# Kernel optimization log

Hardware: AMD Instinct MI355X
Metric: run time of the kernel (lower is better)

Reference implementation:

```python
import jax, jax.numpy as jnp
import numpy as np

NU, NI, D, E = 50000, 100000, 128, 500000
UMAX, IMAX = 50, 50
SQRT_D = float(np.sqrt(D))


def seg_softmax(vals, seg, n):
    # numerically stable softmax over edges grouped by segment id (sparse row softmax)
    m = jax.ops.segment_max(vals, seg, num_segments=n)
    ex = jnp.exp(vals - m[seg])
    s = jax.ops.segment_sum(ex, seg, num_segments=n)
    return ex / s[seg]


def setup_inputs() -> dict:
    key = jax.random.key(0)
    ks = jax.random.split(key, 20)
    w = lambda k: jax.random.normal(k, (D, D), dtype=jnp.float32) * 0.05
    return {
        "u_emb": jax.random.normal(ks[0], (NU, D), dtype=jnp.float32),
        "i_emb": jax.random.normal(ks[1], (NI, D), dtype=jnp.float32),
        "edge_u": jax.random.randint(ks[2], (E,), 0, NU),
        "edge_i": jax.random.randint(ks[3], (E,), 0, NI),
        "rui": jax.random.randint(ks[4], (E,), 0, UMAX),
        "riu": jax.random.randint(ks[5], (E,), 0, IMAX),
        "last_u_items": jax.random.randint(ks[6], (NU,), 0, NI),
        "last_i_users": jax.random.randint(ks[7], (NU,), 0, NU),
        "W1": w(ks[8]), "W2": w(ks[9]), "W1b": w(ks[10]), "W2b": w(ks[11]),
        "W3": w(ks[12]), "W4": w(ks[13]),
        "pV": jax.random.normal(ks[14], (UMAX, D), dtype=jnp.float32),
        "pK": jax.random.normal(ks[15], (IMAX, D), dtype=jnp.float32),
        "last_user_table": jax.random.normal(ks[16], (NU, D), dtype=jnp.float32),
        "last_item_table": jax.random.normal(ks[17], (NI, D), dtype=jnp.float32),
    }


def reference(u_emb, i_emb, edge_u, edge_i, rui, riu, last_u_items, last_i_users,
              W1, W2, W1b, W2b, W3, W4, pV, pK, last_user_table, last_item_table):
    # nn.Linear: y = x @ W.T
    um = u_emb @ W2.T            # (NU, D) user messages
    im = i_emb @ W1.T            # (NI, D) item messages
    um_e = um[edge_u]            # (E, D) gathered per edge
    im_e = im[edge_i]            # (E, D)

    # ---- long term ----
    # dense e = um @ im.T masked to edges == per-edge dot products (same math)
    e_vals = jnp.sum(um_e * im_e, axis=-1)                     # (E,)
    pVui = pV[rui]                                             # (E, D)
    pKiu = pK[riu]                                             # (E, D)
    e_ui = e_vals + jnp.sum(um_e * pVui, axis=-1)
    e_iu = e_vals + jnp.sum(im_e * pKiu, axis=-1)
    alphas = seg_softmax(e_ui / SQRT_D, edge_u, NU)            # softmax over items per user
    betas = seg_softmax(e_iu / SQRT_D, edge_i, NI)             # softmax over users per item

    umb = u_emb @ W2b.T
    imb = i_emb @ W1b.T
    # pass_messages: out[row] = sum_e alpha_e * (messages[col_e] + p_e)
    hLu = jax.ops.segment_sum(alphas[:, None] * (imb[edge_i] + pKiu), edge_u, num_segments=NU)
    hLi = jax.ops.segment_sum(betas[:, None] * (umb[edge_u] + pVui), edge_i, num_segments=NI)

    # ---- short term ----
    li = last_item_table[last_u_items] @ W3.T                  # (NU, D)
    lu = last_user_table[last_i_users] @ W4.T                  # (NU, D)
    a_vals = jnp.sum(li[edge_u] * im_e, axis=-1)               # (E,)
    b_vals = jnp.sum(lu[edge_u] * im_e, axis=-1)               # (E,)
    alphas_s = seg_softmax(a_vals / SQRT_D, edge_u, NU)
    betas_s = seg_softmax(b_vals / SQRT_D, edge_i, NI)
    # p = ones -> messages + 1
    hSu = jax.ops.segment_sum(alphas_s[:, None] * (im_e + 1.0), edge_u, num_segments=NU)
    hSi = jax.ops.segment_sum(betas_s[:, None] * (um_e + 1.0), edge_i, num_segments=NI)

    return (hLu, hSu, hLi, hSi)
```

## Files before the change

### kernel.cpp

```cpp
#include <hip/hip_runtime.h>
#include <hip/hip_bf16.h>
#include <math.h>

#define D_ 128
#define INV_SQRT_D 0.08838834764831845f
#define SCAN_CH 16
#define SCAN_TILE (256 * SCAN_CH)

typedef __bf16 bf16x8 __attribute__((ext_vector_type(8)));
typedef float f32x4 __attribute__((ext_vector_type(4)));

struct W4p { const float* p[4]; };

__device__ __forceinline__ void unpack8(bf16x8 v, float* f) {
    const uint32_t* u = (const uint32_t*)&v;
#pragma unroll
    for (int i = 0; i < 4; i++) {
        uint32_t w = u[i];
        f[2 * i]     = __uint_as_float(w << 16);
        f[2 * i + 1] = __uint_as_float(w & 0xffff0000u);
    }
}

__device__ __forceinline__ bf16x8 pack8(const float* f, float s) {
    bf16x8 r;
#pragma unroll
    for (int j = 0; j < 8; j++) r[j] = (__bf16)(f[j] * s);
    return r;
}

__global__ __launch_bounds__(256) void cvt_weights4(W4p w, __bf16* __restrict__ out) {
    int idx = blockIdx.x * 256 + threadIdx.x;
    if (idx >= 4 * 16384) return;
    out[idx] = (__bf16)w.p[idx >> 14][idx & 16383];
}

__global__ __launch_bounds__(256) void cvt2(const float* __restrict__ a, const float* __restrict__ b,
                                            __bf16* __restrict__ oa, __bf16* __restrict__ ob, int n) {
    int idx = blockIdx.x * 256 + threadIdx.x;
    if (idx < n) { oa[idx] = (__bf16)a[idx]; ob[idx] = (__bf16)b[idx]; }
}

__global__ __launch_bounds__(256) void cvt_emb(const float* __restrict__ u, const float* __restrict__ i,
                                               __bf16* __restrict__ ub, __bf16* __restrict__ ib,
                                               size_t nue, size_t nie) {
    size_t idx4 = ((size_t)blockIdx.x * 256 + threadIdx.x) * 4;
    if (idx4 < nue) {
        float4 v = *(const float4*)(u + idx4);
        ub[idx4] = (__bf16)v.x; ub[idx4+1] = (__bf16)v.y; ub[idx4+2] = (__bf16)v.z; ub[idx4+3] = (__bf16)v.w;
    } else if (idx4 < nue + nie) {
        size_t j = idx4 - nue;
        float4 v = *(const float4*)(i + j);
        ib[j] = (__bf16)v.x; ib[j+1] = (__bf16)v.y; ib[j+2] = (__bf16)v.z; ib[j+3] = (__bf16)v.w;
    }
}

__global__ __launch_bounds__(128) void prep_mats(const float* __restrict__ W1, const float* __restrict__ W2,
                                                 const float* __restrict__ W3, const float* __restrict__ W4,
                                                 const float* __restrict__ pV, const float* __restrict__ pK,
                                                 __bf16* __restrict__ M2t, __bf16* __restrict__ M3t,
                                                 __bf16* __restrict__ M4t,
                                                 __bf16* __restrict__ pVW2, __bf16* __restrict__ pKW1,
                                                 int umax, int imax) {
    __shared__ float sh[256];
    int b = blockIdx.x, t = threadIdx.x;
    if (b < 128) {
        sh[t] = W1[t * 128 + b];
        __syncthreads();
        float m2 = 0.f, m3 = 0.f, m4 = 0.f;
        for (int k = 0; k < 128; k++) {
            float w = sh[k];
            m2 = fmaf(w, W2[k * 128 + t], m2);
            m3 = fmaf(w, W3[k * 128 + t], m3);
            m4 = fmaf(w, W4[k * 128 + t], m4);
        }
        M2t[b * 128 + t] = (__bf16)(m2 * INV_SQRT_D);
        M3t[b * 128 + t] = (__bf16)(m3 * INV_SQRT_D);
        M4t[b * 128 + t] = (__bf16)(m4 * INV_SQRT_D);
    } else {
        int r = b - 128;
        if (r < umax) sh[t] = pV[r * 128 + t];
        if (r < imax) sh[128 + t] = pK[r * 128 + t];
        __syncthreads();
        float q = 0.f, qk = 0.f;
        for (int a = 0; a < 128; a++) {
            if (r < umax) q  = fmaf(sh[a], W2[a * 128 + t], q);
            if (r < imax) qk = fmaf(sh[128 + a], W1[a * 128 + t], qk);
        }
        if (r < umax) pVW2[r * 128 + t] = (__bf16)(q * INV_SQRT_D);
        if (r < imax) pKW1[r * 128 + t] = (__bf16)(qk * INV_SQRT_D);
    }
}

__global__ __launch_bounds__(256) void user_vecs(const float* __restrict__ u_emb,
                                                 const float* __restrict__ lit_tab, const int* __restrict__ g_li,
                                                 const float* __restrict__ lut_tab, const int* __restrict__ g_lu,
                                                 const __bf16* __restrict__ M2t, const __bf16* __restrict__ M3t,
                                                 const __bf16* __restrict__ M4t,
                                                 __bf16* __restrict__ um_t, __bf16* __restrict__ li_t,
                                                 __bf16* __restrict__ lu_t, int rows) {
    int lane = threadIdx.x & 63;
    int wave = threadIdx.x >> 6;
    int row0 = blockIdx.x * 64 + wave * 16;
    if (row0 >= rows) return;
    int l16 = lane & 15, kh = lane >> 4;
    int ar = row0 + l16;
    int arc = ar < rows ? ar : rows - 1;
    const float* rA = u_emb + (size_t)arc * D_;
    const float* rB = lit_tab + (size_t)g_li[arc] * D_;
    const float* rC = lut_tab + (size_t)g_lu[arc] * D_;

    f32x4 aA[8] = {}, aB[8] = {}, aC[8] = {};
#pragma unroll
    for (int k0 = 0; k0 < D_; k0 += 32) {
        int kk = k0 + kh * 8;
        float4 a0 = *(const float4*)(rA + kk), a1 = *(const float4*)(rA + kk + 4);
        float4 b0 = *(const float4*)(rB + kk), b1 = *(const float4*)(rB + kk + 4);
        float4 c0 = *(const float4*)(rC + kk), c1 = *(const float4*)(rC + kk + 4);
        bf16x8 fA, fB, fC;
        fA[0]=(__bf16)a0.x; fA[1]=(__bf16)a0.y; fA[2]=(__bf16)a0.z; fA[3]=(__bf16)a0.w;
        fA[4]=(__bf16)a1.x; fA[5]=(__bf16)a1.y; fA[6]=(__bf16)a1.z; fA[7]=(__bf16)a1.w;
        fB[0]=(__bf16)b0.x; fB[1]=(__bf16)b0.y; fB[2]=(__bf16)b0.z; fB[3]=(__bf16)b0.w;
        fB[4]=(__bf16)b1.x; fB[5]=(__bf16)b1.y; fB[6]=(__bf16)b1.z; fB[7]=(__bf16)b1.w;
        fC[0]=(__bf16)c0.x; fC[1]=(__bf16)c0.y; fC[2]=(__bf16)c0.z; fC[3]=(__bf16)c0.w;
        fC[4]=(__bf16)c1.x; fC[5]=(__bf16)c1.y; fC[6]=(__bf16)c1.z; fC[7]=(__bf16)c1.w;
#pragma unroll
        for (int cb = 0; cb < 8; cb++) {
            bf16x8 w2 = *(const bf16x8*)(M2t + (size_t)(cb * 16 + l16) * D_ + kk);
            aA[cb] = __builtin_amdgcn_mfma_f32_16x16x32_bf16(fA, w2, aA[cb], 0, 0, 0);
            bf16x8 w3 = *(const bf16x8*)(M3t + (size_t)(cb * 16 + l16) * D_ + kk);
            aB[cb] = __builtin_amdgcn_mfma_f32_16x16x32_bf16(fB, w3, aB[cb], 0, 0, 0);
            bf16x8 w4 = *(const bf16x8*)(M4t + (size_t)(cb * 16 + l16) * D_ + kk);
            aC[cb] = __builtin_amdgcn_mfma_f32_16x16x32_bf16(fC, w4, aC[cb], 0, 0, 0);
        }
    }
#pragma unroll
    for (int cb = 0; cb < 8; cb++) {
#pragma unroll
        for (int j = 0; j < 4; j++) {
            int r = row0 + kh * 4 + j;
            if (r < rows) {
                um_t[(size_t)r * D_ + cb * 16 + l16] = (__bf16)aA[cb][j];
                li_t[(size_t)r * D_ + cb * 16 + l16] = (__bf16)aB[cb][j];
                lu_t[(size_t)r * D_ + cb * 16 + l16] = (__bf16)aC[cb][j];
            }
        }
    }
}

__global__ __launch_bounds__(256) void gemm_pvk(const __bf16* __restrict__ Xb,
                                                const __bf16* __restrict__ Pb,
                                                float* __restrict__ Y, int rows, int ncols) {
    int lane = threadIdx.x & 63;
    int wave = threadIdx.x >> 6;
    int row0 = blockIdx.x * 64 + wave * 16;
    if (row0 >= rows) return;
    int l16 = lane & 15, kh = lane >> 4;
    int ar = row0 + l16;
    int arc = ar < rows ? ar : rows - 1;
    const __bf16* arow = Xb + (size_t)arc * D_;

    f32x4 acc[4] = {};
#pragma unroll
    for (int k0 = 0; k0 < D_; k0 += 32) {
        int kk = k0 + kh * 8;
        bf16x8 af = *(const bf16x8*)(arow + kk);
#pragma unroll
        for (int cb = 0; cb < 4; cb++) {
            int br = cb * 16 + l16;
            if (br >= ncols) br = ncols - 1;
            bf16x8 bf = *(const bf16x8*)(Pb + (size_t)br * D_ + kk);
            acc[cb] = __builtin_amdgcn_mfma_f32_16x16x32_bf16(af, bf, acc[cb], 0, 0, 0);
        }
    }
#pragma unroll
    for (int cb = 0; cb < 4; cb++) {
        int col = cb * 16 + l16;
        if (col >= ncols) continue;
#pragma unroll
        for (int j = 0; j < 4; j++) {
            int r = row0 + kh * 4 + j;
            if (r < rows) Y[(size_t)r * ncols + col] = acc[cb][j];
        }
    }
}

__global__ __launch_bounds__(256) void hist2(const int* __restrict__ eu, const int* __restrict__ ei,
                                             int* __restrict__ cnt_all, int nu, int E) {
    int e = blockIdx.x * 256 + threadIdx.x;
    if (e < E) {
        atomicAdd(&cnt_all[eu[e]], 1);
        atomicAdd(&cnt_all[nu + ei[e]], 1);
    }
}

__global__ __launch_bounds__(256) void scan_phaseA(const int* __restrict__ cnt, int* __restrict__ part, int n) {
    __shared__ int wsum[4];
    int t = threadIdx.x, lane = t & 63, w = t >> 6;
    int i0 = blockIdx.x * SCAN_TILE + t * SCAN_CH;
    int tot = 0;
#pragma unroll
    for (int j = 0; j < SCAN_CH; j++) tot += (i0 + j < n) ? cnt[i0 + j] : 0;
#pragma unroll
    for (int d = 32; d; d >>= 1) tot += __shfl_xor(tot, d);
    if (lane == 0) wsum[w] = tot;
    __syncthreads();
    if (t == 0) part[blockIdx.x] = wsum[0] + wsum[1] + wsum[2] + wsum[3];
}

__global__ __launch_bounds__(1024) void scan_phaseB(int* __restrict__ part, int nb,
                                                    int* __restrict__ off, int n) {
    __shared__ int wsum[16];
    int t = threadIdx.x, lane = t & 63, w = t >> 6;
    int v = (t < nb) ? part[t] : 0;
    int x = v;
#pragma unroll
    for (int d = 1; d < 64; d <<= 1) {
        int y = __shfl_up(x, d);
        if (lane >= d) x += y;
    }
    if (lane == 63) wsum[w] = x;
    __syncthreads();
    int wbase = 0;
    for (int ww = 0; ww < w; ww++) wbase += wsum[ww];
    if (t < nb) part[t] = wbase + x - v;
    if (t == 1023) off[n] = wbase + x;
}

__global__ __launch_bounds__(256) void scan_phaseC(const int* __restrict__ cnt, const int* __restrict__ part,
                                                   int* __restrict__ off, int* __restrict__ pos, int n) {
    __shared__ int wsum[4];
    int t = threadIdx.x, lane = t & 63, w = t >> 6;
    int i0 = blockIdx.x * SCAN_TILE + t * SCAN_CH;
    int loc[SCAN_CH];
    int tot = 0;
#pragma unroll
    for (int j = 0; j < SCAN_CH; j++) {
        int v = (i0 + j < n) ? cnt[i0 + j] : 0;
        loc[j] = tot; tot += v;
    }
    int x = tot;
#pragma unroll
    for (int d = 1; d < 64; d <<= 1) {
        int y = __shfl_up(x, d);
        if (lane >= d) x += y;
    }
    if (lane == 63) wsum[w] = x;
    __syncthreads();
    int wbase = 0;
    for (int ww = 0; ww < w; ww++) wbase += wsum[ww];
    int excl = part[blockIdx.x] + wbase + x - tot;
#pragma unroll
    for (int j = 0; j < SCAN_CH; j++) {
        if (i0 + j < n) { off[i0 + j] = excl + loc[j]; pos[i0 + j] = excl + loc[j]; }
    }
}

__global__ __launch_bounds__(256) void scatter2(const int* __restrict__ eu, const int* __restrict__ ei,
                                                const int* __restrict__ rui, const int* __restrict__ riu,
                                                int* __restrict__ pos_all, int4* __restrict__ recs,
                                                int nu, int E) {
    int e = blockIdx.x * 256 + threadIdx.x;
    if (e < E) {
        int u = eu[e], it = ei[e], r1 = rui[e], r2 = riu[e];
        int pi = atomicAdd(&pos_all[nu + it], 1);
        int pu = atomicAdd(&pos_all[u], 1);
        recs[pu] = make_int4(it, r1, r2, pi);
        recs[pi] = make_int4(u, r1, r2, 0);
    }
}

__global__ __launch_bounds__(256) void user_pass(const int* __restrict__ off_all, const int4* __restrict__ recs,
                                                 const __bf16* __restrict__ ib_emb,
                                                 const __bf16* __restrict__ um_t,
                                                 const __bf16* __restrict__ li_t,
                                                 const __bf16* __restrict__ lu_t,
                                                 const __bf16* __restrict__ pKb,
                                                 const float* __restrict__ upv,
                                                 float2* __restrict__ mb_val,
                                                 __bf16* __restrict__ A1n, __bf16* __restrict__ PKn,
                                                 __bf16* __restrict__ A2n, int nu, int umax) {
    int u = blockIdx.x * 4 + (threadIdx.x >> 6);
    if (u >= nu) return;
    int lane = threadIdx.x & 63;
    int g = lane >> 4, l16 = lane & 15;
    int off = off_all[u], n = off_all[u + 1] - off;
    if (n == 0) {
        if (lane < 16) {
            bf16x8 z = {};
            *(bf16x8*)(A1n + (size_t)u * D_ + l16 * 8) = z;
            *(bf16x8*)(PKn + (size_t)u * D_ + l16 * 8) = z;
            *(bf16x8*)(A2n + (size_t)u * D_ + l16 * 8) = z;
        }
        return;
    }
    float um8[8], li8[8], lu8[8];
    unpack8(((const bf16x8*)(um_t + (size_t)u * D_))[l16], um8);
    unpack8(((const bf16x8*)(li_t + (size_t)u * D_))[l16], li8);
    unpack8(((const bf16x8*)(lu_t + (size_t)u * D_))[l16], lu8);
    const float* upv_row = upv + (size_t)u * umax;

    float s1 = 0.f, s2 = 0.f, a1[8] = {}, apk[8] = {}, a2[8] = {};
    for (int i = g; i < n; i += 8) {
        int4 ra = recs[off + i];
        bool hb = (i + 4) < n;
        int4 rb = recs[off + (hb ? i + 4 : i)];
        bf16x8 vieA = ((const bf16x8*)(ib_emb + (size_t)ra.x * D_))[l16];
        bf16x8 vpkA = ((const bf16x8*)(pKb + (size_t)ra.z * D_))[l16];
        bf16x8 vieB = ((const bf16x8*)(ib_emb + (size_t)rb.x * D_))[l16];
        bf16x8 vpkB = ((const bf16x8*)(pKb + (size_t)rb.z * D_))[l16];
        float fieA[8], fpkA[8], fieB[8], fpkB[8];
        unpack8(vieA, fieA); unpack8(vpkA, fpkA);
        unpack8(vieB, fieB); unpack8(vpkB, fpkB);
        float d1a = 0.f, d2a = 0.f, d3a = 0.f, d1b = 0.f, d2b = 0.f, d3b = 0.f;
#pragma unroll
        for (int j = 0; j < 8; j++) {
            d1a = fmaf(um8[j], fieA[j], d1a);
            d2a = fmaf(li8[j], fieA[j], d2a);
            d3a = fmaf(lu8[j], fieA[j], d3a);
            d1b = fmaf(um8[j], fieB[j], d1b);
            d2b = fmaf(li8[j], fieB[j], d2b);
            d3b = fmaf(lu8[j], fieB[j], d3b);
        }
#pragma unroll
        for (int d = 1; d < 16; d <<= 1) {
            d1a += __shfl_xor(d1a, d); d2a += __shfl_xor(d2a, d); d3a += __shfl_xor(d3a, d);
            d1b += __shfl_xor(d1b, d); d2b += __shfl_xor(d2b, d); d3b += __shfl_xor(d3b, d);
        }
        if (l16 == 0) {
            mb_val[ra.w] = make_float2(d1a, d3a);
            if (hb) mb_val[rb.w] = make_float2(d1b, d3b);
        }
        float w1a = __expf(d1a + upv_row[ra.y]);
        float w2a = __expf(d2a);
        float w1b = hb ? __expf(d1b + upv_row[rb.y]) : 0.f;
        float w2b = hb ? __expf(d2b) : 0.f;
        s1 += w1a + w1b; s2 += w2a + w2b;
#pragma unroll
        for (int j = 0; j < 8; j++) {
            a1[j]  = fmaf(w1a, fieA[j], fmaf(w1b, fieB[j], a1[j]));
            apk[j] = fmaf(w1a, fpkA[j], fmaf(w1b, fpkB[j], apk[j]));
            a2[j]  = fmaf(w2a, fieA[j], fmaf(w2b, fieB[j], a2[j]));
        }
    }
#pragma unroll
    for (int d = 16; d < 64; d <<= 1) {
        s1 += __shfl_xor(s1, d); s2 += __shfl_xor(s2, d);
#pragma unroll
        for (int j = 0; j < 8; j++) {
            a1[j]  += __shfl_xor(a1[j], d);
            apk[j] += __shfl_xor(apk[j], d);
            a2[j]  += __shfl_xor(a2[j], d);
        }
    }
    if (lane < 16) {
        float inv1 = 1.f / s1, inv2 = 1.f / s2;
        *(bf16x8*)(A1n + (size_t)u * D_ + l16 * 8) = pack8(a1, inv1);
        *(bf16x8*)(PKn + (size_t)u * D_ + l16 * 8) = pack8(apk, inv1);
        *(bf16x8*)(A2n + (size_t)u * D_ + l16 * 8) = pack8(a2, inv2);
    }
}

__global__ __launch_bounds__(256) void item_pass(const int* __restrict__ off_all, const int4* __restrict__ recs,
                                                 const __bf16* __restrict__ ub_emb,
                                                 const __bf16* __restrict__ pVb,
                                                 const float* __restrict__ ipk,
                                                 const float2* __restrict__ mb_val,
                                                 __bf16* __restrict__ B1n, __bf16* __restrict__ PVn,
                                                 __bf16* __restrict__ B2n, int nu, int ni, int imax) {
    int it = blockIdx.x * 4 + (threadIdx.x >> 6);
    if (it >= ni) return;
    int lane = threadIdx.x & 63;
    int g = lane >> 4, l16 = lane & 15;
    int off = off_all[nu + it], n = off_all[nu + it + 1] - off;
    if (n == 0) {
        if (lane < 16) {
            bf16x8 z = {};
            *(bf16x8*)(B1n + (size_t)it * D_ + l16 * 8) = z;
            *(bf16x8*)(PVn + (size_t)it * D_ + l16 * 8) = z;
            *(bf16x8*)(B2n + (size_t)it * D_ + l16 * 8) = z;
        }
        return;
    }
    const float* ipk_row = ipk + (size_t)it * imax;

    float s1 = 0.f, s2 = 0.f, b1[8] = {}, bpv[8] = {}, b2[8] = {};
    for (int i = g; i < n; i += 8) {
        int4 ra = recs[off + i];
        bool hb = (i + 4) < n;
        int4 rb = recs[off + (hb ? i + 4 : i)];
        float2 ma = mb_val[off + i];
        float2 mbv = hb ? mb_val[off + i + 4] : make_float2(0.f, 0.f);
        bf16x8 vueA = ((const bf16x8*)(ub_emb + (size_t)ra.x * D_))[l16];
        bf16x8 vpvA = ((const bf16x8*)(pVb + (size_t)ra.y * D_))[l16];
        bf16x8 vueB = ((const bf16x8*)(ub_emb + (size_t)rb.x * D_))[l16];
        bf16x8 vpvB = ((const bf16x8*)(pVb + (size_t)rb.y * D_))[l16];
        float fueA[8], fpvA[8], fueB[8], fpvB[8];
        unpack8(vueA, fueA); unpack8(vpvA, fpvA);
        unpack8(vueB, fueB); unpack8(vpvB, fpvB);
        float w1a = __expf(ma.x + ipk_row[ra.z]);
        float w2a = __expf(ma.y);
        float w1b = hb ? __expf(mbv.x + ipk_row[rb.z]) : 0.f;
        float w2b = hb ? __expf(mbv.y) : 0.f;
        s1 += w1a + w1b; s2 += w2a + w2b;
#pragma unroll
        for (int j = 0; j < 8; j++) {
            b1[j]  = fmaf(w1a, fueA[j], fmaf(w1b, fueB[j], b1[j]));
            bpv[j] = fmaf(w1a, fpvA[j], fmaf(w1b, fpvB[j], bpv[j]));
            b2[j]  = fmaf(w2a, fueA[j], fmaf(w2b, fueB[j], b2[j]));
        }
    }
#pragma unroll
    for (int d = 16; d < 64; d <<= 1) {
        s1 += __shfl_xor(s1, d); s2 += __shfl_xor(s2, d);
#pragma unroll
        for (int j = 0; j < 8; j++) {
            b1[j]  += __shfl_xor(b1[j], d);
            bpv[j] += __shfl_xor(bpv[j], d);
            b2[j]  += __shfl_xor(b2[j], d);
        }
    }
    if (lane < 16) {
        float inv1 = 1.f / s1, inv2 = 1.f / s2;
        *(bf16x8*)(B1n + (size_t)it * D_ + l16 * 8) = pack8(b1, inv1);
        *(bf16x8*)(PVn + (size_t)it * D_ + l16 * 8) = pack8(bpv, inv1);
        *(bf16x8*)(B2n + (size_t)it * D_ + l16 * 8) = pack8(b2, inv2);
    }
}

__global__ __launch_bounds__(256) void finish1(const __bf16* __restrict__ A, const __bf16* __restrict__ Wsrc,
                                               const __bf16* __restrict__ side, const int* __restrict__ offseg,
                                               float* __restrict__ out, int rows) {
    __shared__ __bf16 sW[128][136];
    __shared__ float stg[4][16][132];
    int t = threadIdx.x;
#pragma unroll
    for (int it = 0; it < 8; it++) {
        int slot = it * 256 + t;
        int r = slot >> 4, c16 = (slot & 15) * 8;
        bf16x8 v = *(const bf16x8*)(Wsrc + (size_t)r * D_ + c16);
        *(bf16x8*)(&sW[r][c16]) = v;
    }
    __syncthreads();
    int lane = t & 63, wave = t >> 6;
    int l16 = lane & 15, kh = lane >> 4;
    int hw = lane >> 5, c4 = (lane & 31) * 4;

    for (int tt = 0; tt < 4; tt++) {
        int row0 = blockIdx.x * 256 + (tt * 4 + wave) * 16;
        if (row0 >= rows) break;
        int ar = row0 + l16;
        int arc = ar < rows ? ar : rows - 1;
        const __bf16* rA = A + (size_t)arc * D_;
        bf16x8 a0 = *(const bf16x8*)(rA + kh * 8);
        bf16x8 a1 = *(const bf16x8*)(rA + 32 + kh * 8);
        bf16x8 a2 = *(const bf16x8*)(rA + 64 + kh * 8);
        bf16x8 a3 = *(const bf16x8*)(rA + 96 + kh * 8);
        f32x4 acc[8] = {};
#pragma unroll
        for (int cb = 0; cb < 8; cb++) {
            int wr = cb * 16 + l16;
            acc[cb] = __builtin_amdgcn_mfma_f32_16x16x32_bf16(a0, *(const bf16x8*)(&sW[wr][kh * 8]), acc[cb], 0, 0, 0);
            acc[cb] = __builtin_amdgcn_mfma_f32_16x16x32_bf16(a1, *(const bf16x8*)(&sW[wr][32 + kh * 8]), acc[cb], 0, 0, 0);
            acc[cb] = __builtin_amdgcn_mfma_f32_16x16x32_bf16(a2, *(const bf16x8*)(&sW[wr][64 + kh * 8]), acc[cb], 0, 0, 0);
            acc[cb] = __builtin_amdgcn_mfma_f32_16x16x32_bf16(a3, *(const bf16x8*)(&sW[wr][96 + kh * 8]), acc[cb], 0, 0, 0);
        }
#pragma unroll
        for (int cb = 0; cb < 8; cb++)
#pragma unroll
            for (int j = 0; j < 4; j++)
                stg[wave][kh * 4 + j][cb * 16 + l16] = acc[cb][j];
#pragma unroll
        for (int k = 0; k < 8; k++) {
            int wr = hw + k * 2;
            int rg = row0 + wr;
            if (rg < rows) {
                float4 v = *(const float4*)&stg[wave][wr][c4];
                if (side) {
                    ushort4 sv = *(const ushort4*)((const unsigned short*)side + (size_t)rg * D_ + c4);
                    v.x += __uint_as_float((uint32_t)sv.x << 16);
                    v.y += __uint_as_float((uint32_t)sv.y << 16);
                    v.z += __uint_as_float((uint32_t)sv.z << 16);
                    v.w += __uint_as_float((uint32_t)sv.w << 16);
                } else {
                    float one = (offseg[rg + 1] - offseg[rg]) > 0 ? 1.f : 0.f;
                    v.x += one; v.y += one; v.z += one; v.w += one;
                }
                *(float4*)(out + (size_t)rg * D_ + c4) = v;
            }
        }
    }
}

extern "C" void kernel_launch(void* const* d_in, const int* in_sizes, int n_in,
                              void* d_out, int out_size, void* d_ws, size_t ws_size,
                              hipStream_t stream) {
    (void)n_in; (void)out_size; (void)ws_size;
    const float* u_emb = (const float*)d_in[0];
    const float* i_emb = (const float*)d_in[1];
    const int* edge_u = (const int*)d_in[2];
    const int* edge_i = (const int*)d_in[3];
    const int* rui = (const int*)d_in[4];
    const int* riu = (const int*)d_in[5];
    const int* last_u_items = (const int*)d_in[6];
    const int* last_i_users = (const int*)d_in[7];
    const float* W1  = (const float*)d_in[8];
    const float* W2  = (const float*)d_in[9];
    const float* W1b = (const float*)d_in[10];
    const float* W2b = (const float*)d_in[11];
    const float* W3  = (const float*)d_in[12];
    const float* W4  = (const float*)d_in[13];
    const float* pV  = (const float*)d_in[14];
    const float* pK  = (const float*)d_in[15];
    const float* last_user_table = (const float*)d_in[16];
    const float* last_item_table = (const float*)d_in[17];

    const int NU = in_sizes[0] / D_;
    const int NI = in_sizes[1] / D_;
    const int E  = in_sizes[2];
    const int UMAXr = in_sizes[14] / D_;
    const int IMAXr = in_sizes[15] / D_;
    const int NSEG = NU + NI;

    size_t cur = 0;
    auto alloc = [&](size_t bytes) -> void* {
        void* p = (char*)d_ws + cur;
        cur += (bytes + 255) & ~(size_t)255;
        return p;
    };

    __bf16* Wb4   = (__bf16*)alloc(4 * 16384 * 2);
    __bf16* M2t   = (__bf16*)alloc(16384 * 2);
    __bf16* M3t   = (__bf16*)alloc(16384 * 2);
    __bf16* M4t   = (__bf16*)alloc(16384 * 2);
    __bf16* pVW2  = (__bf16*)alloc((size_t)UMAXr * D_ * 2);
    __bf16* pKW1  = (__bf16*)alloc((size_t)IMAXr * D_ * 2);
    __bf16* pVb   = (__bf16*)alloc((size_t)UMAXr * D_ * 2);
    __bf16* pKb   = (__bf16*)alloc((size_t)IMAXr * D_ * 2);
    __bf16* ub_emb = (__bf16*)alloc((size_t)NU * D_ * 2);
    __bf16* ib_emb = (__bf16*)alloc((size_t)NI * D_ * 2);
    __bf16* um_t  = (__bf16*)alloc((size_t)NU * D_ * 2);
    __bf16* li_t  = (__bf16*)alloc((size_t)NU * D_ * 2);
    __bf16* lu_t  = (__bf16*)alloc((size_t)NU * D_ * 2);
    float* upv    = (float*)alloc((size_t)NU * UMAXr * 4);
    float* ipk    = (float*)alloc((size_t)NI * IMAXr * 4);
    __bf16* A1n   = (__bf16*)alloc((size_t)NU * D_ * 2);
    __bf16* PKn   = (__bf16*)alloc((size_t)NU * D_ * 2);
    __bf16* A2n   = (__bf16*)alloc((size_t)NU * D_ * 2);
    __bf16* B1n   = (__bf16*)alloc((size_t)NI * D_ * 2);
    __bf16* PVn   = (__bf16*)alloc((size_t)NI * D_ * 2);
    __bf16* B2n   = (__bf16*)alloc((size_t)NI * D_ * 2);
    float2* mb_val = (float2*)alloc((size_t)2 * E * 8);
    int4* recs    = (int4*)alloc((size_t)2 * E * 16);
    int* cnt_all  = (int*)alloc((size_t)NSEG * 4);
    int* off_all  = (int*)alloc((size_t)(NSEG + 1) * 4);
    int* pos_all  = (int*)alloc((size_t)NSEG * 4);
    int* parts    = (int*)alloc(1024 * 4);

    float* out = (float*)d_out;
    float* hLu = out;
    float* hSu = out + (size_t)NU * D_;
    float* hLi = out + (size_t)2 * NU * D_;
    float* hSi = out + (size_t)2 * NU * D_ + (size_t)NI * D_;

    W4p w4; w4.p[0] = W1; w4.p[1] = W2; w4.p[2] = W1b; w4.p[3] = W2b;
    cvt_weights4<<<(4 * 16384 + 255) / 256, 256, 0, stream>>>(w4, Wb4);
    prep_mats<<<128 + (UMAXr > IMAXr ? UMAXr : IMAXr), 128, 0, stream>>>(W1, W2, W3, W4, pV, pK,
                                                                         M2t, M3t, M4t, pVW2, pKW1, UMAXr, IMAXr);
    cvt2<<<(UMAXr * D_ + 255) / 256, 256, 0, stream>>>(pV, pK, pVb, pKb, UMAXr * D_);
    size_t nue = (size_t)NU * D_, nie = (size_t)NI * D_;
    cvt_emb<<<(int)(((nue + nie) / 4 + 255) / 256), 256, 0, stream>>>(u_emb, i_emb, ub_emb, ib_emb, nue, nie);

    hipMemsetAsync(cnt_all, 0, (size_t)NSEG * 4, stream);
    hist2<<<(E + 255) / 256, 256, 0, stream>>>(edge_u, edge_i, cnt_all, NU, E);
    int nb = (NSEG + SCAN_TILE - 1) / SCAN_TILE;
    scan_phaseA<<<nb, 256, 0, stream>>>(cnt_all, parts, NSEG);
    scan_phaseB<<<1, 1024, 0, stream>>>(parts, nb, off_all, NSEG);
    scan_phaseC<<<nb, 256, 0, stream>>>(cnt_all, parts, off_all, pos_all, NSEG);
    scatter2<<<(E + 255) / 256, 256, 0, stream>>>(edge_u, edge_i, rui, riu, pos_all, recs, NU, E);

    int gu = (NU + 63) / 64, gi = (NI + 63) / 64;
    user_vecs<<<gu, 256, 0, stream>>>(u_emb, last_item_table, last_u_items, last_user_table, last_i_users,
                                      M2t, M3t, M4t, um_t, li_t, lu_t, NU);
    gemm_pvk<<<gu, 256, 0, stream>>>(ub_emb, pVW2, upv, NU, UMAXr);
    gemm_pvk<<<gi, 256, 0, stream>>>(ib_emb, pKW1, ipk, NI, IMAXr);

    user_pass<<<(NU + 3) / 4, 256, 0, stream>>>(off_all, recs, ib_emb, um_t, li_t, lu_t,
                                                pKb, upv, mb_val, A1n, PKn, A2n, NU, UMAXr);
    item_pass<<<(NI + 3) / 4, 256, 0, stream>>>(off_all, recs, ub_emb, pVb, ipk, mb_val,
                                                B1n, PVn, B2n, NU, NI, IMAXr);

    int fu = (NU + 255) / 256, fi = (NI + 255) / 256;
    finish1<<<fu, 256, 0, stream>>>(A1n, Wb4 + 2 * 16384, PKn, nullptr, hLu, NU);
    finish1<<<fu, 256, 0, stream>>>(A2n, Wb4 + 0 * 16384, nullptr, off_all, hSu, NU);
    finish1<<<fi, 256, 0, stream>>>(B1n, Wb4 + 3 * 16384, PVn, nullptr, hLi, NI);
    finish1<<<fi, 256, 0, stream>>>(B2n, Wb4 + 1 * 16384, nullptr, off_all + NU, hSi, NI);
}
```

Baseline: 557.4 us.

## Pack edge records into bit-packed compact lists and merge small convert kernels

Replaces the 16-byte int4 CSR edge records with bit-packed lists: users get an int2 holding the item id with both relation indices folded into the upper bits plus the item-side position, and items get a single int. The item-side offsets are shifted by E so mb_val shrinks to E entries. This cuts scatter write traffic and per-edge index load bandwidth in both aggregation passes. It also fuses the weight and pV/pK bf16 conversion kernels into one launch. The encoding assumes ids below 2^18 and relation indices below 64, which holds for these sizes but is a hard limit.

```diff
diff --git a/kernel.cpp b/kernel.cpp
--- a/kernel.cpp
+++ b/kernel.cpp
@@ -29,16 +29,19 @@
     return r;
 }
 
-__global__ __launch_bounds__(256) void cvt_weights4(W4p w, __bf16* __restrict__ out) {
+__global__ __launch_bounds__(256) void cvt_small(W4p w, const float* __restrict__ pV, const float* __restrict__ pK,
+                                                 __bf16* __restrict__ outW, __bf16* __restrict__ pVb,
+                                                 __bf16* __restrict__ pKb, int npv, int npk) {
     int idx = blockIdx.x * 256 + threadIdx.x;
-    if (idx >= 4 * 16384) return;
-    out[idx] = (__bf16)w.p[idx >> 14][idx & 16383];
-}
-
-__global__ __launch_bounds__(256) void cvt2(const float* __restrict__ a, const float* __restrict__ b,
-                                            __bf16* __restrict__ oa, __bf16* __restrict__ ob, int n) {
-    int idx = blockIdx.x * 256 + threadIdx.x;
-    if (idx < n) { oa[idx] = (__bf16)a[idx]; ob[idx] = (__bf16)b[idx]; }
+    if (idx < 4 * 16384) {
+        outW[idx] = (__bf16)w.p[idx >> 14][idx & 16383];
+    } else if (idx - 4 * 16384 < npv) {
+        int j = idx - 4 * 16384;
+        pVb[j] = (__bf16)pV[j];
+    } else if (idx - 4 * 16384 - npv < npk) {
+        int j = idx - 4 * 16384 - npv;
+        pKb[j] = (__bf16)pK[j];
+    }
 }
 
 __global__ __launch_bounds__(256) void cvt_emb(const float* __restrict__ u, const float* __restrict__ i,
@@ -258,19 +261,20 @@
 
 __global__ __launch_bounds__(256) void scatter2(const int* __restrict__ eu, const int* __restrict__ ei,
                                                 const int* __restrict__ rui, const int* __restrict__ riu,
-                                                int* __restrict__ pos_all, int4* __restrict__ recs,
-                                                int nu, int E) {
+                                                int* __restrict__ pos_all, int2* __restrict__ u_list,
+                                                int* __restrict__ i_list, int nu, int E) {
     int e = blockIdx.x * 256 + threadIdx.x;
     if (e < E) {
         int u = eu[e], it = ei[e], r1 = rui[e], r2 = riu[e];
-        int pi = atomicAdd(&pos_all[nu + it], 1);
+        int rbits = (r1 << 18) | (r2 << 24);
+        int pi = atomicAdd(&pos_all[nu + it], 1) - E;
         int pu = atomicAdd(&pos_all[u], 1);
-        recs[pu] = make_int4(it, r1, r2, pi);
-        recs[pi] = make_int4(u, r1, r2, 0);
-    }
-}
-
-__global__ __launch_bounds__(256) void user_pass(const int* __restrict__ off_all, const int4* __restrict__ recs,
+        u_list[pu] = make_int2(it | rbits, pi);
+        i_list[pi] = u | rbits;
+    }
+}
+
+__global__ __launch_bounds__(256) void user_pass(const int* __restrict__ off_all, const int2* __restrict__ u_list,
                                                  const __bf16* __restrict__ ib_emb,
                                                  const __bf16* __restrict__ um_t,
                                                  const __bf16* __restrict__ li_t,
@@ -302,13 +306,15 @@
 
     float s1 = 0.f, s2 = 0.f, a1[8] = {}, apk[8] = {}, a2[8] = {};
     for (int i = g; i < n; i += 8) {
-        int4 ra = recs[off + i];
+        int2 ra = u_list[off + i];
         bool hb = (i + 4) < n;
-        int4 rb = recs[off + (hb ? i + 4 : i)];
-        bf16x8 vieA = ((const bf16x8*)(ib_emb + (size_t)ra.x * D_))[l16];
-        bf16x8 vpkA = ((const bf16x8*)(pKb + (size_t)ra.z * D_))[l16];
-        bf16x8 vieB = ((const bf16x8*)(ib_emb + (size_t)rb.x * D_))[l16];
-        bf16x8 vpkB = ((const bf16x8*)(pKb + (size_t)rb.z * D_))[l16];
+        int2 rb = u_list[off + (hb ? i + 4 : i)];
+        int itA = ra.x & 0x3FFFF, r1A = (ra.x >> 18) & 0x3F, r2A = (ra.x >> 24) & 0x3F;
+        int itB = rb.x & 0x3FFFF, r1B = (rb.x >> 18) & 0x3F, r2B = (rb.x >> 24) & 0x3F;
+        bf16x8 vieA = ((const bf16x8*)(ib_emb + (size_t)itA * D_))[l16];
+        bf16x8 vpkA = ((const bf16x8*)(pKb + (size_t)r2A * D_))[l16];
+        bf16x8 vieB = ((const bf16x8*)(ib_emb + (size_t)itB * D_))[l16];
+        bf16x8 vpkB = ((const bf16x8*)(pKb + (size_t)r2B * D_))[l16];
         float fieA[8], fpkA[8], fieB[8], fpkB[8];
         unpack8(vieA, fieA); unpack8(vpkA, fpkA);
         unpack8(vieB, fieB); unpack8(vpkB, fpkB);
@@ -328,12 +334,12 @@
             d1b += __shfl_xor(d1b, d); d2b += __shfl_xor(d2b, d); d3b += __shfl_xor(d3b, d);
         }
         if (l16 == 0) {
-            mb_val[ra.w] = make_float2(d1a, d3a);
-            if (hb) mb_val[rb.w] = make_float2(d1b, d3b);
-        }
-        float w1a = __expf(d1a + upv_row[ra.y]);
+            mb_val[ra.y] = make_float2(d1a, d3a);
+            if (hb) mb_val[rb.y] = make_float2(d1b, d3b);
+        }
+        float w1a = __expf(d1a + upv_row[r1A]);
         float w2a = __expf(d2a);
-        float w1b = hb ? __expf(d1b + upv_row[rb.y]) : 0.f;
+        float w1b = hb ? __expf(d1b + upv_row[r1B]) : 0.f;
         float w2b = hb ? __expf(d2b) : 0.f;
         s1 += w1a + w1b; s2 += w2a + w2b;
 #pragma unroll
@@ -361,18 +367,18 @@
     }
 }
 
-__global__ __launch_bounds__(256) void item_pass(const int* __restrict__ off_all, const int4* __restrict__ recs,
+__global__ __launch_bounds__(256) void item_pass(const int* __restrict__ off_all, const int* __restrict__ i_list,
                                                  const __bf16* __restrict__ ub_emb,
                                                  const __bf16* __restrict__ pVb,
                                                  const float* __restrict__ ipk,
                                                  const float2* __restrict__ mb_val,
                                                  __bf16* __restrict__ B1n, __bf16* __restrict__ PVn,
-                                                 __bf16* __restrict__ B2n, int nu, int ni, int imax) {
+                                                 __bf16* __restrict__ B2n, int nu, int ni, int imax, int E) {
     int it = blockIdx.x * 4 + (threadIdx.x >> 6);
     if (it >= ni) return;
     int lane = threadIdx.x & 63;
     int g = lane >> 4, l16 = lane & 15;
-    int off = off_all[nu + it], n = off_all[nu + it + 1] - off;
+    int ioff = off_all[nu + it] - E, n = off_all[nu + it + 1] - E - ioff;
     if (n == 0) {
         if (lane < 16) {
             bf16x8 z = {};
@@ -386,21 +392,23 @@
 
     float s1 = 0.f, s2 = 0.f, b1[8] = {}, bpv[8] = {}, b2[8] = {};
     for (int i = g; i < n; i += 8) {
-        int4 ra = recs[off + i];
+        int pa = i_list[ioff + i];
         bool hb = (i + 4) < n;
-        int4 rb = recs[off + (hb ? i + 4 : i)];
-        float2 ma = mb_val[off + i];
-        float2 mbv = hb ? mb_val[off + i + 4] : make_float2(0.f, 0.f);
-        bf16x8 vueA = ((const bf16x8*)(ub_emb + (size_t)ra.x * D_))[l16];
-        bf16x8 vpvA = ((const bf16x8*)(pVb + (size_t)ra.y * D_))[l16];
-        bf16x8 vueB = ((const bf16x8*)(ub_emb + (size_t)rb.x * D_))[l16];
-        bf16x8 vpvB = ((const bf16x8*)(pVb + (size_t)rb.y * D_))[l16];
+        int pb = i_list[ioff + (hb ? i + 4 : i)];
+        int uA = pa & 0x3FFFF, r1A = (pa >> 18) & 0x3F, r2A = (pa >> 24) & 0x3F;
+        int uB = pb & 0x3FFFF, r1B = (pb >> 18) & 0x3F, r2B = (pb >> 24) & 0x3F;
+        float2 ma = mb_val[ioff + i];
+        float2 mbv = hb ? mb_val[ioff + i + 4] : make_float2(0.f, 0.f);
+        bf16x8 vueA = ((const bf16x8*)(ub_emb + (size_t)uA * D_))[l16];
+        bf16x8 vpvA = ((const bf16x8*)(pVb + (size_t)r1A * D_))[l16];
+        bf16x8 vueB = ((const bf16x8*)(ub_emb + (size_t)uB * D_))[l16];
+        bf16x8 vpvB = ((const bf16x8*)(pVb + (size_t)r1B * D_))[l16];
         float fueA[8], fpvA[8], fueB[8], fpvB[8];
         unpack8(vueA, fueA); unpack8(vpvA, fpvA);
         unpack8(vueB, fueB); unpack8(vpvB, fpvB);
-        float w1a = __expf(ma.x + ipk_row[ra.z]);
+        float w1a = __expf(ma.x + ipk_row[r2A]);
         float w2a = __expf(ma.y);
-        float w1b = hb ? __expf(mbv.x + ipk_row[rb.z]) : 0.f;
+        float w1b = hb ? __expf(mbv.x + ipk_row[r2B]) : 0.f;
         float w2b = hb ? __expf(mbv.y) : 0.f;
         s1 += w1a + w1b; s2 += w2a + w2b;
 #pragma unroll
@@ -550,8 +558,9 @@
     __bf16* B1n   = (__bf16*)alloc((size_t)NI * D_ * 2);
     __bf16* PVn   = (__bf16*)alloc((size_t)NI * D_ * 2);
     __bf16* B2n   = (__bf16*)alloc((size_t)NI * D_ * 2);
-    float2* mb_val = (float2*)alloc((size_t)2 * E * 8);
-    int4* recs    = (int4*)alloc((size_t)2 * E * 16);
+    float2* mb_val = (float2*)alloc((size_t)E * 8);
+    int2* u_list  = (int2*)alloc((size_t)E * 8);
+    int* i_list   = (int*)alloc((size_t)E * 4);
     int* cnt_all  = (int*)alloc((size_t)NSEG * 4);
     int* off_all  = (int*)alloc((size_t)(NSEG + 1) * 4);
     int* pos_all  = (int*)alloc((size_t)NSEG * 4);
@@ -564,10 +573,10 @@
     float* hSi = out + (size_t)2 * NU * D_ + (size_t)NI * D_;
 
     W4p w4; w4.p[0] = W1; w4.p[1] = W2; w4.p[2] = W1b; w4.p[3] = W2b;
-    cvt_weights4<<<(4 * 16384 + 255) / 256, 256, 0, stream>>>(w4, Wb4);
+    int npv = UMAXr * D_, npk = IMAXr * D_;
+    cvt_small<<<(4 * 16384 + npv + npk + 255) / 256, 256, 0, stream>>>(w4, pV, pK, Wb4, pVb, pKb, npv, npk);
     prep_mats<<<128 + (UMAXr > IMAXr ? UMAXr : IMAXr), 128, 0, stream>>>(W1, W2, W3, W4, pV, pK,
                                                                          M2t, M3t, M4t, pVW2, pKW1, UMAXr, IMAXr);
-    cvt2<<<(UMAXr * D_ + 255) / 256, 256, 0, stream>>>(pV, pK, pVb, pKb, UMAXr * D_);
     size_t nue = (size_t)NU * D_, nie = (size_t)NI * D_;
     cvt_emb<<<(int)(((nue + nie) / 4 + 255) / 256), 256, 0, stream>>>(u_emb, i_emb, ub_emb, ib_emb, nue, nie);
 
@@ -577,7 +586,7 @@
     scan_phaseA<<<nb, 256, 0, stream>>>(cnt_all, parts, NSEG);
     scan_phaseB<<<1, 1024, 0, stream>>>(parts, nb, off_all, NSEG);
     scan_phaseC<<<nb, 256, 0, stream>>>(cnt_all, parts, off_all, pos_all, NSEG);
-    scatter2<<<(E + 255) / 256, 256, 0, stream>>>(edge_u, edge_i, rui, riu, pos_all, recs, NU, E);
+    scatter2<<<(E + 255) / 256, 256, 0, stream>>>(edge_u, edge_i, rui, riu, pos_all, u_list, i_list, NU, E);
 
     int gu = (NU + 63) / 64, gi = (NI + 63) / 64;
     user_vecs<<<gu, 256, 0, stream>>>(u_emb, last_item_table, last_u_items, last_user_table, last_i_users,
@@ -585,10 +594,10 @@
     gemm_pvk<<<gu, 256, 0, stream>>>(ub_emb, pVW2, upv, NU, UMAXr);
     gemm_pvk<<<gi, 256, 0, stream>>>(ib_emb, pKW1, ipk, NI, IMAXr);
 
-    user_pass<<<(NU + 3) / 4, 256, 0, stream>>>(off_all, recs, ib_emb, um_t, li_t, lu_t,
+    user_pass<<<(NU + 3) / 4, 256, 0, stream>>>(off_all, u_list, ib_emb, um_t, li_t, lu_t,
                                                 pKb, upv, mb_val, A1n, PKn, A2n, NU, UMAXr);
-    item_pass<<<(NI + 3) / 4, 256, 0, stream>>>(off_all, recs, ub_emb, pVb, ipk, mb_val,
-                                                B1n, PVn, B2n, NU, NI, IMAXr);
+    item_pass<<<(NI + 3) / 4, 256, 0, stream>>>(off_all, i_list, ub_emb, pVb, ipk, mb_val,
+                                                B1n, PVn, B2n, NU, NI, IMAXr, E);
 
     int fu = (NU + 255) / 256, fi = (NI + 255) / 256;
     finish1<<<fu, 256, 0, stream>>>(A1n, Wb4 + 2 * 16384, PKn, nullptr, hLu, NU);
```

New measurement: 541.2 us. 2.9% less time.
